# Performance work log

Hardware: AMD Instinct MI355X
Metric: run time of the kernel (lower is better)

## Reference

```python
import jax, jax.numpy as jnp
import numpy as np

SEQ, BATCH, IN_DIM, HID = 512, 4096, 1, 30

def setup_inputs() -> dict:
    key = jax.random.key(0)
    ks = jax.random.split(key, 7)
    s = 1.0 / np.sqrt(HID)  # PyTorch RNN/Linear init scale
    X = jax.random.normal(ks[0], (SEQ, BATCH, IN_DIM), dtype=jnp.float32)
    W_ih = jax.random.uniform(ks[1], (HID, IN_DIM), jnp.float32, -s, s)
    W_hh = jax.random.uniform(ks[2], (HID, HID), jnp.float32, -s, s)
    b_ih = jax.random.uniform(ks[3], (HID,), jnp.float32, -s, s)
    b_hh = jax.random.uniform(ks[4], (HID,), jnp.float32, -s, s)
    W_out = jax.random.uniform(ks[5], (1, HID), jnp.float32, -s, s)
    b_out = jax.random.uniform(ks[6], (1,), jnp.float32, -s, s)
    return {"X": X, "W_ih": W_ih, "W_hh": W_hh, "b_ih": b_ih,
            "b_hh": b_hh, "W_out": W_out, "b_out": b_out}

def reference(X, W_ih, W_hh, b_ih, b_hh, W_out, b_out):
    # X: [S, B, 1]. Module transposes to batch_first [B, S, 1], runs tanh RNN,
    # applies Linear(30->1), transposes back -> [S, B, 1].
    S, B, _ = X.shape
    # Precompute input projection for all timesteps (input_size=1 -> cheap).
    x_proj = jnp.einsum('sbi,hi->sbh', X, W_ih) + b_ih + b_hh  # [S, B, H]
    h0 = jnp.zeros((B, W_hh.shape[0]), dtype=X.dtype)

    def step(h, xp):
        h_new = jnp.tanh(xp + h @ W_hh.T)
        return h_new, h_new

    _, hs = jax.lax.scan(step, h0, x_proj)  # hs: [S, B, H]
    y = jnp.einsum('sbh,oh->sbo', hs, W_out) + b_out  # [S, B, 1]
    return y
```

## Files before the change

kernel.cpp:

```cpp
#include <hip/hip_runtime.h>


#define SEQ 512
#define BATCH 4096
#define HID 30

__global__ __launch_bounds__(256, 2) void rnn_tanh_kernel(
    const float* __restrict__ X,
    const float* __restrict__ W_ih,
    const float* __restrict__ W_hh,
    const float* __restrict__ b_ih,
    const float* __restrict__ b_hh,
    const float* __restrict__ W_out,
    const float* __restrict__ b_out,
    float* __restrict__ Y)
{
  const int tid  = threadIdx.x;
  const int lane = tid & 31;
  const int g    = tid >> 5;
  const int gb   = blockIdx.x * 8 + g;

  __shared__ float hlds[8][32];

  float wih = 0.f, bsum = 0.f;
  float wrow[HID];
#pragma unroll
  for (int j = 0; j < HID; ++j) wrow[j] = 0.f;
  if (lane < HID) {
    wih  = W_ih[lane];
    bsum = b_ih[lane] + b_hh[lane];
#pragma unroll
    for (int j = 0; j < HID; ++j) wrow[j] = W_hh[lane * HID + j];
  } else if (lane == HID) {
    bsum = b_out[0];
#pragma unroll
    for (int j = 0; j < HID; ++j) wrow[j] = W_out[j];
  }
#pragma unroll
  for (int j = 0; j < HID; ++j) asm volatile("" : "+v"(wrow[j]));
  asm volatile("" : "+v"(wih));
  asm volatile("" : "+v"(bsum));

  hlds[g][lane] = 0.f;
  const float* hp = &hlds[g][0];

  float4 hv0 = *reinterpret_cast<const float4*>(hp + 0);
  float4 hv1 = *reinterpret_cast<const float4*>(hp + 4);
  float4 hv2 = *reinterpret_cast<const float4*>(hp + 8);
  float4 hv3 = *reinterpret_cast<const float4*>(hp + 12);
  float4 hv4 = *reinterpret_cast<const float4*>(hp + 16);
  float4 hv5 = *reinterpret_cast<const float4*>(hp + 20);
  float4 hv6 = *reinterpret_cast<const float4*>(hp + 24);
  float2 hv7 = *reinterpret_cast<const float2*>(hp + 28);

  float x0 = X[0 * BATCH + gb];
  float x1 = X[1 * BATCH + gb];
  float x2 = X[2 * BATCH + gb];
  float x3 = X[3 * BATCH + gb];

  auto FMA_PASS = [&](float init) -> float {
    float a0 = init, a1 = 0.f, a2 = 0.f, a3 = 0.f;
    a0 = fmaf(wrow[0],  hv0.x, a0); a1 = fmaf(wrow[1],  hv0.y, a1);
    a2 = fmaf(wrow[2],  hv0.z, a2); a3 = fmaf(wrow[3],  hv0.w, a3);
    a0 = fmaf(wrow[4],  hv1.x, a0); a1 = fmaf(wrow[5],  hv1.y, a1);
    a2 = fmaf(wrow[6],  hv1.z, a2); a3 = fmaf(wrow[7],  hv1.w, a3);
    a0 = fmaf(wrow[8],  hv2.x, a0); a1 = fmaf(wrow[9],  hv2.y, a1);
    a2 = fmaf(wrow[10], hv2.z, a2); a3 = fmaf(wrow[11], hv2.w, a3);
    a0 = fmaf(wrow[12], hv3.x, a0); a1 = fmaf(wrow[13], hv3.y, a1);
    a2 = fmaf(wrow[14], hv3.z, a2); a3 = fmaf(wrow[15], hv3.w, a3);
    a0 = fmaf(wrow[16], hv4.x, a0); a1 = fmaf(wrow[17], hv4.y, a1);
    a2 = fmaf(wrow[18], hv4.z, a2); a3 = fmaf(wrow[19], hv4.w, a3);
    a0 = fmaf(wrow[20], hv5.x, a0); a1 = fmaf(wrow[21], hv5.y, a1);
    a2 = fmaf(wrow[22], hv5.z, a2); a3 = fmaf(wrow[23], hv5.w, a3);
    a0 = fmaf(wrow[24], hv6.x, a0); a1 = fmaf(wrow[25], hv6.y, a1);
    a2 = fmaf(wrow[26], hv6.z, a2); a3 = fmaf(wrow[27], hv6.w, a3);
    a0 = fmaf(wrow[28], hv7.x, a0); a1 = fmaf(wrow[29], hv7.y, a1);
    return (a0 + a1) + (a2 + a3);
  };

  auto STEP = [&](int s, float& xreg) {
    float acc = FMA_PASS(fmaf(xreg, wih, bsum));
    const int snext = (s + 4 < SEQ) ? s + 4 : SEQ - 1;
    xreg = X[snext * BATCH + gb];

    if (lane == HID && s != 0) Y[(s - 1) * BATCH + gb] = acc;

    const float t = __builtin_amdgcn_fmed3f(acc, -9.f, 9.f);
    const float e = __builtin_amdgcn_exp2f(t * 2.885390081777927f);
    const float h = fmaf(-2.f, __builtin_amdgcn_rcpf(e + 1.f), 1.f);

    hlds[g][lane] = h;
    hv0 = *reinterpret_cast<const float4*>(hp + 0);
    hv1 = *reinterpret_cast<const float4*>(hp + 4);
    hv2 = *reinterpret_cast<const float4*>(hp + 8);
    hv3 = *reinterpret_cast<const float4*>(hp + 12);
    hv4 = *reinterpret_cast<const float4*>(hp + 16);
    hv5 = *reinterpret_cast<const float4*>(hp + 20);
    hv6 = *reinterpret_cast<const float4*>(hp + 24);
    hv7 = *reinterpret_cast<const float2*>(hp + 28);
  };

  for (int s = 0; s < SEQ; s += 4) {
    STEP(s + 0, x0);
    STEP(s + 1, x1);
    STEP(s + 2, x2);
    STEP(s + 3, x3);
  }

  const float ylast = FMA_PASS(bsum);
  if (lane == HID) Y[(SEQ - 1) * BATCH + gb] = ylast;
}

extern "C" void kernel_launch(void* const* d_in, const int* in_sizes, int n_in,
                              void* d_out, int out_size, void* d_ws, size_t ws_size,
                              hipStream_t stream) {
  const float* X     = (const float*)d_in[0];
  const float* W_ih  = (const float*)d_in[1];
  const float* W_hh  = (const float*)d_in[2];
  const float* b_ih  = (const float*)d_in[3];
  const float* b_hh  = (const float*)d_in[4];
  const float* W_out = (const float*)d_in[5];
  const float* b_out = (const float*)d_in[6];
  float* Y = (float*)d_out;

  dim3 grid(BATCH / 8), block(256);
  rnn_tanh_kernel<<<grid, block, 0, stream>>>(X, W_ih, W_hh, b_ih, b_hh,
                                              W_out, b_out, Y);
}
```

Measured before the change: 100.5 us.

## Split each hidden dot product across wave halves with cross-half shuffle reduction

Each 64-lane wavefront now handles one batch element instead of two, with the two 32-lane halves each computing half of the 30-term recurrent dot product and combining via a xor-32 shuffle. This halves the per-lane weight registers and the per-step LDS reads and FMA chain, shortening the serial critical path of every timestep. In exchange the grid doubles, raising waves per SIMD and adding a cross-lane shuffle plus duplicated tanh work each step.

```diff
diff --git a/kernel.cpp b/kernel.cpp
--- a/kernel.cpp
+++ b/kernel.cpp
@@ -5,7 +5,7 @@
 #define BATCH 4096
 #define HID 30
 
-__global__ __launch_bounds__(256, 2) void rnn_tanh_kernel(
+__global__ __launch_bounds__(256, 4) void rnn_tanh_kernel(
     const float* __restrict__ X,
     const float* __restrict__ W_ih,
     const float* __restrict__ W_hh,
@@ -16,72 +16,76 @@
     float* __restrict__ Y)
 {
   const int tid  = threadIdx.x;
-  const int lane = tid & 31;
-  const int g    = tid >> 5;
-  const int gb   = blockIdx.x * 8 + g;
+  const int lane = tid & 63;
+  const int j    = lane & 31;
+  const int half = lane >> 5;
+  const int wid  = tid >> 6;
+  const int gb   = __builtin_amdgcn_readfirstlane(blockIdx.x * 4 + wid);
 
-  __shared__ float hlds[8][32];
+  __shared__ float hlds[4][32];
 
   float wih = 0.f, bsum = 0.f;
-  float wrow[HID];
+  float w[16];
 #pragma unroll
-  for (int j = 0; j < HID; ++j) wrow[j] = 0.f;
-  if (lane < HID) {
-    wih  = W_ih[lane];
-    bsum = b_ih[lane] + b_hh[lane];
+  for (int k = 0; k < 16; ++k) w[k] = 0.f;
+
+  if (j < HID) {
+    if (half == 0) {
+      wih  = W_ih[j];
+      bsum = b_ih[j] + b_hh[j];
 #pragma unroll
-    for (int j = 0; j < HID; ++j) wrow[j] = W_hh[lane * HID + j];
-  } else if (lane == HID) {
-    bsum = b_out[0];
+      for (int k = 0; k < 16; ++k) w[k] = W_hh[j * HID + k];
+    } else {
 #pragma unroll
-    for (int j = 0; j < HID; ++j) wrow[j] = W_out[j];
+      for (int k = 0; k < 14; ++k) w[k] = W_hh[j * HID + 16 + k];
+    }
+  } else if (j == HID) {
+    if (half == 0) {
+      bsum = b_out[0];
+#pragma unroll
+      for (int k = 0; k < 16; ++k) w[k] = W_out[k];
+    } else {
+#pragma unroll
+      for (int k = 0; k < 14; ++k) w[k] = W_out[16 + k];
+    }
   }
 #pragma unroll
-  for (int j = 0; j < HID; ++j) asm volatile("" : "+v"(wrow[j]));
-  asm volatile("" : "+v"(wih));
-  asm volatile("" : "+v"(bsum));
+  for (int k = 0; k < 16; ++k) asm volatile("" : "+v"(w[k]));
+  asm volatile("" : "+v"(wih), "+v"(bsum));
 
-  hlds[g][lane] = 0.f;
-  const float* hp = &hlds[g][0];
+  hlds[wid][j] = 0.f;
+  const float* hp = &hlds[wid][half * 16];
 
   float4 hv0 = *reinterpret_cast<const float4*>(hp + 0);
   float4 hv1 = *reinterpret_cast<const float4*>(hp + 4);
   float4 hv2 = *reinterpret_cast<const float4*>(hp + 8);
   float4 hv3 = *reinterpret_cast<const float4*>(hp + 12);
-  float4 hv4 = *reinterpret_cast<const float4*>(hp + 16);
-  float4 hv5 = *reinterpret_cast<const float4*>(hp + 20);
-  float4 hv6 = *reinterpret_cast<const float4*>(hp + 24);
-  float2 hv7 = *reinterpret_cast<const float2*>(hp + 28);
 
-  float x0 = X[0 * BATCH + gb];
-  float x1 = X[1 * BATCH + gb];
-  float x2 = X[2 * BATCH + gb];
-  float x3 = X[3 * BATCH + gb];
+  const float* Xg = X + gb;
+  float x0 = Xg[0 * BATCH];
+  float x1 = Xg[1 * BATCH];
+  float x2 = Xg[2 * BATCH];
+  float x3 = Xg[3 * BATCH];
 
   auto FMA_PASS = [&](float init) -> float {
     float a0 = init, a1 = 0.f, a2 = 0.f, a3 = 0.f;
-    a0 = fmaf(wrow[0],  hv0.x, a0); a1 = fmaf(wrow[1],  hv0.y, a1);
-    a2 = fmaf(wrow[2],  hv0.z, a2); a3 = fmaf(wrow[3],  hv0.w, a3);
-    a0 = fmaf(wrow[4],  hv1.x, a0); a1 = fmaf(wrow[5],  hv1.y, a1);
-    a2 = fmaf(wrow[6],  hv1.z, a2); a3 = fmaf(wrow[7],  hv1.w, a3);
-    a0 = fmaf(wrow[8],  hv2.x, a0); a1 = fmaf(wrow[9],  hv2.y, a1);
-    a2 = fmaf(wrow[10], hv2.z, a2); a3 = fmaf(wrow[11], hv2.w, a3);
-    a0 = fmaf(wrow[12], hv3.x, a0); a1 = fmaf(wrow[13], hv3.y, a1);
-    a2 = fmaf(wrow[14], hv3.z, a2); a3 = fmaf(wrow[15], hv3.w, a3);
-    a0 = fmaf(wrow[16], hv4.x, a0); a1 = fmaf(wrow[17], hv4.y, a1);
-    a2 = fmaf(wrow[18], hv4.z, a2); a3 = fmaf(wrow[19], hv4.w, a3);
-    a0 = fmaf(wrow[20], hv5.x, a0); a1 = fmaf(wrow[21], hv5.y, a1);
-    a2 = fmaf(wrow[22], hv5.z, a2); a3 = fmaf(wrow[23], hv5.w, a3);
-    a0 = fmaf(wrow[24], hv6.x, a0); a1 = fmaf(wrow[25], hv6.y, a1);
-    a2 = fmaf(wrow[26], hv6.z, a2); a3 = fmaf(wrow[27], hv6.w, a3);
-    a0 = fmaf(wrow[28], hv7.x, a0); a1 = fmaf(wrow[29], hv7.y, a1);
+    a0 = fmaf(w[0],  hv0.x, a0); a1 = fmaf(w[1],  hv0.y, a1);
+    a2 = fmaf(w[2],  hv0.z, a2); a3 = fmaf(w[3],  hv0.w, a3);
+    a0 = fmaf(w[4],  hv1.x, a0); a1 = fmaf(w[5],  hv1.y, a1);
+    a2 = fmaf(w[6],  hv1.z, a2); a3 = fmaf(w[7],  hv1.w, a3);
+    a0 = fmaf(w[8],  hv2.x, a0); a1 = fmaf(w[9],  hv2.y, a1);
+    a2 = fmaf(w[10], hv2.z, a2); a3 = fmaf(w[11], hv2.w, a3);
+    a0 = fmaf(w[12], hv3.x, a0); a1 = fmaf(w[13], hv3.y, a1);
+    a2 = fmaf(w[14], hv3.z, a2); a3 = fmaf(w[15], hv3.w, a3);
     return (a0 + a1) + (a2 + a3);
   };
 
   auto STEP = [&](int s, float& xreg) {
-    float acc = FMA_PASS(fmaf(xreg, wih, bsum));
+    const float part = FMA_PASS(fmaf(xreg, wih, bsum));
     const int snext = (s + 4 < SEQ) ? s + 4 : SEQ - 1;
-    xreg = X[snext * BATCH + gb];
+    xreg = Xg[snext * BATCH];
+
+    const float acc = part + __shfl_xor(part, 32, 64);
 
     if (lane == HID && s != 0) Y[(s - 1) * BATCH + gb] = acc;
 
@@ -89,15 +93,11 @@
     const float e = __builtin_amdgcn_exp2f(t * 2.885390081777927f);
     const float h = fmaf(-2.f, __builtin_amdgcn_rcpf(e + 1.f), 1.f);
 
-    hlds[g][lane] = h;
+    hlds[wid][j] = h;
     hv0 = *reinterpret_cast<const float4*>(hp + 0);
     hv1 = *reinterpret_cast<const float4*>(hp + 4);
     hv2 = *reinterpret_cast<const float4*>(hp + 8);
     hv3 = *reinterpret_cast<const float4*>(hp + 12);
-    hv4 = *reinterpret_cast<const float4*>(hp + 16);
-    hv5 = *reinterpret_cast<const float4*>(hp + 20);
-    hv6 = *reinterpret_cast<const float4*>(hp + 24);
-    hv7 = *reinterpret_cast<const float2*>(hp + 28);
   };
 
   for (int s = 0; s < SEQ; s += 4) {
@@ -107,8 +107,9 @@
     STEP(s + 3, x3);
   }
 
-  const float ylast = FMA_PASS(bsum);
-  if (lane == HID) Y[(SEQ - 1) * BATCH + gb] = ylast;
+  const float part = FMA_PASS(bsum);
+  const float acc = part + __shfl_xor(part, 32, 64);
+  if (lane == HID) Y[(SEQ - 1) * BATCH + gb] = acc;
 }
 
 extern "C" void kernel_launch(void* const* d_in, const int* in_sizes, int n_in,
@@ -123,7 +124,7 @@
   const float* b_out = (const float*)d_in[6];
   float* Y = (float*)d_out;
 
-  dim3 grid(BATCH / 8), block(256);
+  dim3 grid(BATCH / 4), block(256);
   rnn_tanh_kernel<<<grid, block, 0, stream>>>(X, W_ih, W_hh, b_ih, b_hh,
                                               W_out, b_out, Y);
 }
```

New measurement: 198.9 us. 97.8% more time.
